# Kernel tuning notes

Hardware: AMD Instinct MI355X
Metric: run time of the kernel (lower is better)

Reference implementation:

```python
import jax, jax.numpy as jnp
import numpy as np

NEG_INF = -1e30  # stand-in for -inf, avoids NaN under masked rows edge cases


def setup_inputs() -> dict:
    key = jax.random.key(0)
    ks = jax.random.split(key, 6)
    H, N, F_IN, HD, F_OUT = 8, 4096, 512, 64, 512
    X = jax.random.normal(ks[0], (H, N, F_IN), dtype=jnp.float32)
    mask = jax.random.randint(ks[1], (H, N, N), 0, 2, dtype=jnp.int32)
    s = 1.0 / np.sqrt(F_IN)
    W_Q = jax.random.normal(ks[2], (H, HD, F_IN), dtype=jnp.float32) * s
    W_K = jax.random.normal(ks[3], (H, HD, F_IN), dtype=jnp.float32) * s
    W_V = jax.random.normal(ks[4], (H, HD, F_IN), dtype=jnp.float32) * s
    W_O = jax.random.normal(ks[5], (F_OUT, H * HD), dtype=jnp.float32) * (1.0 / np.sqrt(H * HD))
    return {"X": X, "mask": mask, "W_Q": W_Q, "W_K": W_K, "W_V": W_V, "W_O": W_O}


def reference(X, mask, W_Q, W_K, W_V, W_O):
    # X: [H, N, F_in]; W_{Q,K,V}: [H, head_dim, F_in] (torch Linear layout: [out,in])
    Q = jnp.einsum('hnf,hdf->hnd', X, W_Q)
    K = jnp.einsum('hnf,hdf->hnd', X, W_K)
    V = jnp.einsum('hnf,hdf->hnd', X, W_V)
    head_dim = K.shape[-1]
    E = jnp.einsum('hnd,hmd->hnm', Q, K) / jnp.sqrt(jnp.float32(head_dim))  # [H,N,N]
    E = jnp.where(mask == 0, jnp.float32(NEG_INF), E)
    A = jax.nn.softmax(E, axis=-1)
    Hout = jnp.einsum('hnm,hmd->hnd', A, V)  # [H, N, head_dim]
    # concat heads along feature dim -> [N, H*head_dim]
    Hcat = jnp.transpose(Hout, (1, 0, 2)).reshape(Hout.shape[1], -1)
    # dropout is identity in eval mode
    return Hcat @ W_O.T  # [N, fan_out]
```

## Files before the change

### kernel.cpp

```cpp
#include <hip/hip_runtime.h>

typedef __bf16 bf16x8 __attribute__((ext_vector_type(8)));
typedef float f32x4 __attribute__((ext_vector_type(4)));
typedef int i32x4 __attribute__((ext_vector_type(4)));

#define MFMA(a, b, c) __builtin_amdgcn_mfma_f32_16x16x32_bf16((a), (b), (c), 0, 0, 0)
#define GLOAD_LDS(g, l) __builtin_amdgcn_global_load_lds( \
    (const __attribute__((address_space(1))) void*)(g),   \
    (__attribute__((address_space(3))) void*)(l), 16, 0, 0)

constexpr int HEADS = 8, SEQ = 4096, FIN = 512, HD = 64, FOUT = 512;
constexpr float QSCALE = 0.18033688011112042f;

__device__ inline bf16x8 cvt8(const float* __restrict__ p) {
    f32x4 a = *(const f32x4*)p;
    f32x4 b = *(const f32x4*)(p + 4);
    bf16x8 r;
    r[0] = (__bf16)a[0]; r[1] = (__bf16)a[1]; r[2] = (__bf16)a[2]; r[3] = (__bf16)a[3];
    r[4] = (__bf16)b[0]; r[5] = (__bf16)b[1]; r[6] = (__bf16)b[2]; r[7] = (__bf16)b[3];
    return r;
}

__global__ __launch_bounds__(256) void qkv_kernel(
    const float* __restrict__ X, const float* __restrict__ Wq,
    const float* __restrict__ Wk, const float* __restrict__ Wv,
    __bf16* __restrict__ Q, __bf16* __restrict__ K, __bf16* __restrict__ Vt)
{
    const int h = blockIdx.y;
    const int tid = threadIdx.x;
    const int w = tid >> 6, lane = tid & 63;
    const int quad = lane >> 4, l16 = lane & 15;
    const int m = blockIdx.x * 64 + w * 16 + l16;

    const float* xrow = X + ((size_t)h * SEQ + m) * FIN + quad * 8;
    const float* wqh = Wq + (size_t)h * HD * FIN + quad * 8;
    const float* wkh = Wk + (size_t)h * HD * FIN + quad * 8;
    const float* wvh = Wv + (size_t)h * HD * FIN + quad * 8;

    const f32x4 vzero = {0.f, 0.f, 0.f, 0.f};
    f32x4 accQ[4], accK[4], accV[4];
#pragma unroll
    for (int t = 0; t < 4; ++t) { accQ[t] = vzero; accK[t] = vzero; accV[t] = vzero; }

    for (int f0 = 0; f0 < FIN; f0 += 32) {
        bf16x8 a = cvt8(xrow + f0);
#pragma unroll
        for (int t = 0; t < 4; ++t) {
            const int wrow = (t * 16 + l16) * FIN + f0;
            bf16x8 bq = cvt8(wqh + wrow);
            bf16x8 bk = cvt8(wkh + wrow);
            bf16x8 bv = cvt8(wvh + wrow);
            accQ[t] = MFMA(a, bq, accQ[t]);
            accK[t] = MFMA(a, bk, accK[t]);
            accV[t] = MFMA(a, bv, accV[t]);
        }
    }

    const int row0 = blockIdx.x * 64 + w * 16 + quad * 4;
#pragma unroll
    for (int t = 0; t < 4; ++t) {
        const int d = t * 16 + l16;
#pragma unroll
        for (int r = 0; r < 4; ++r) {
            const int n = row0 + r;
            Q[((size_t)h * SEQ + n) * HD + d] = (__bf16)(accQ[t][r] * QSCALE);
            K[((size_t)h * SEQ + n) * HD + d] = (__bf16)accK[t][r];
            Vt[((size_t)h * HD + d) * SEQ + n] = (__bf16)accV[t][r];
        }
    }
}

__global__ __launch_bounds__(256) void attn_kernel(
    const __bf16* __restrict__ Q, const __bf16* __restrict__ K,
    const __bf16* __restrict__ Vt, const int* __restrict__ mask,
    __bf16* __restrict__ Hcat)
{
    __shared__ __align__(16) unsigned char lds[32768 + 4 * 2048];

    const int bid = blockIdx.x;
    const int h = bid & 7;
    const int q0b = (bid >> 3) * 64;
    const int tid = threadIdx.x;
    const int w = tid >> 6, lane = tid & 63;
    const int quad = lane >> 4, l16 = lane & 15;
    const int q0 = q0b + w * 16;
    const int e7 = l16 & 7;

    __bf16* PT = (__bf16*)(lds + 32768) + w * 1024;

    const __bf16* Qh = Q + (size_t)h * SEQ * HD;
    const __bf16* Kh = K + (size_t)h * SEQ * HD;
    const __bf16* Vh = Vt + (size_t)h * HD * SEQ;
    const int* mrow = mask + ((size_t)h * SEQ + q0 + l16) * SEQ + quad * 4;

    auto stage = [&](int n0, int b) {
        unsigned char* bK = lds + b * 8192;
        unsigned char* bV = lds + 16384 + b * 8192;
#pragma unroll
        for (int c = 0; c < 2; ++c) {
            const int s = c * 256 + w * 64 + lane;
            const int row = s >> 3;
            const int cq = (s & 7) ^ (row & 7);
            GLOAD_LDS(Kh + (size_t)(n0 + row) * HD + cq * 8, bK + (c * 256 + w * 64) * 16);
            GLOAD_LDS(Vh + (size_t)row * SEQ + n0 + cq * 8, bV + (c * 256 + w * 64) * 16);
        }
    };
    auto loadM = [&](int n0, i32x4* mv) {
#pragma unroll
        for (int t = 0; t < 4; ++t) mv[t] = *(const i32x4*)(mrow + n0 + t * 16);
    };

    bf16x8 qa0 = *(const bf16x8*)(Qh + (size_t)(q0 + l16) * HD + quad * 8);
    bf16x8 qa1 = *(const bf16x8*)(Qh + (size_t)(q0 + l16) * HD + 32 + quad * 8);

    const f32x4 vzero = {0.f, 0.f, 0.f, 0.f};
    f32x4 O[4];
    float lsum = 0.f;
#pragma unroll
    for (int t = 0; t < 4; ++t) O[t] = vzero;

    i32x4 mA[4], mB[4];
    stage(0, 0);
    loadM(0, mA);
    __syncthreads();

    auto tile = [&](int i, const i32x4* mc, i32x4* mn) {
        const int n0 = i * 64;
        const int cur = i & 1;
        if (i + 1 < SEQ / 64) {
            stage(n0 + 64, cur ^ 1);
            loadM(n0 + 64, mn);
        }
        const __bf16* cK = (const __bf16*)(lds + cur * 8192);
        const __bf16* cV = (const __bf16*)(lds + 16384 + cur * 8192);

        f32x4 St[4];
#pragma unroll
        for (int t = 0; t < 4; ++t) {
            const int kr = t * 16 + l16;
            bf16x8 kb0 = *(const bf16x8*)(cK + kr * 64 + ((quad ^ (kr & 7)) * 8));
            bf16x8 kb1 = *(const bf16x8*)(cK + kr * 64 + (((quad + 4) ^ (kr & 7)) * 8));
            St[t] = MFMA(kb0, qa0, vzero);
            St[t] = MFMA(kb1, qa1, St[t]);
        }

#pragma unroll
        for (int t = 0; t < 4; ++t) {
            union { unsigned long long u; __bf16 hh[4]; } pk;
#pragma unroll
            for (int r = 0; r < 4; ++r) {
                float p = __builtin_amdgcn_exp2f(St[t][r]);
                p = mc[t][r] ? p : 0.f;
                lsum += p;
                pk.hh[r] = (__bf16)p;
            }
            const int c = t * 2 + (quad >> 1);
            *(unsigned long long*)(PT + l16 * 64 + ((c ^ e7) * 8) + (quad & 1) * 4) = pk.u;
        }

        bf16x8 pa0 = *(const bf16x8*)(PT + l16 * 64 + ((quad ^ e7) * 8));
        bf16x8 pa1 = *(const bf16x8*)(PT + l16 * 64 + (((quad + 4) ^ e7) * 8));
#pragma unroll
        for (int t = 0; t < 4; ++t) {
            const int dr = t * 16 + l16;
            bf16x8 vb0 = *(const bf16x8*)(cV + dr * 64 + ((quad ^ (dr & 7)) * 8));
            bf16x8 vb1 = *(const bf16x8*)(cV + dr * 64 + (((quad + 4) ^ (dr & 7)) * 8));
            O[t] = MFMA(pa0, vb0, O[t]);
            O[t] = MFMA(pa1, vb1, O[t]);
        }
        __syncthreads();
    };

    for (int i = 0; i < SEQ / 64; i += 2) {
        tile(i, mA, mB);
        tile(i + 1, mB, mA);
    }

    lsum += __shfl_xor(lsum, 16, 64);
    lsum += __shfl_xor(lsum, 32, 64);
    float inv[4];
#pragma unroll
    for (int r = 0; r < 4; ++r) {
        float Lr = __shfl(lsum, quad * 4 + r, 64);
        inv[r] = Lr > 0.f ? 1.0f / Lr : 0.f;
    }

#pragma unroll
    for (int r = 0; r < 4; ++r) {
        const int n = q0 + quad * 4 + r;
#pragma unroll
        for (int t = 0; t < 4; ++t)
            Hcat[(size_t)n * FOUT + h * HD + t * 16 + l16] = (__bf16)(O[t][r] * inv[r]);
    }
}

__global__ __launch_bounds__(256) void out_kernel(
    const __bf16* __restrict__ Hcat, const float* __restrict__ Wo,
    float* __restrict__ out)
{
    const int tid = threadIdx.x;
    const int w = tid >> 6, lane = tid & 63;
    const int quad = lane >> 4, l16 = lane & 15;
    const int n0 = blockIdx.x * 64 + w * 16;
    const int o0 = blockIdx.y * 64;

    const f32x4 vzero = {0.f, 0.f, 0.f, 0.f};
    f32x4 acc[4];
#pragma unroll
    for (int t = 0; t < 4; ++t) acc[t] = vzero;

    for (int k0 = 0; k0 < FOUT; k0 += 32) {
        bf16x8 a = *(const bf16x8*)(Hcat + (size_t)(n0 + l16) * FOUT + k0 + quad * 8);
#pragma unroll
        for (int t = 0; t < 4; ++t) {
            bf16x8 b = cvt8(Wo + (size_t)(o0 + t * 16 + l16) * FOUT + k0 + quad * 8);
            acc[t] = MFMA(a, b, acc[t]);
        }
    }
#pragma unroll
    for (int t = 0; t < 4; ++t)
#pragma unroll
        for (int r = 0; r < 4; ++r)
            out[(size_t)(n0 + quad * 4 + r) * FOUT + o0 + t * 16 + l16] = acc[t][r];
}

extern "C" void kernel_launch(void* const* d_in, const int* in_sizes, int n_in,
                              void* d_out, int out_size, void* d_ws, size_t ws_size,
                              hipStream_t stream) {
    const float* X    = (const float*)d_in[0];
    const int*   mask = (const int*)d_in[1];
    const float* Wq   = (const float*)d_in[2];
    const float* Wk   = (const float*)d_in[3];
    const float* Wv   = (const float*)d_in[4];
    const float* Wo   = (const float*)d_in[5];
    float* out = (float*)d_out;

    __bf16* Q    = (__bf16*)d_ws;
    __bf16* K    = Q + (size_t)HEADS * SEQ * HD;
    __bf16* Vt   = K + (size_t)HEADS * SEQ * HD;
    __bf16* Hcat = Vt + (size_t)HEADS * HD * SEQ;

    qkv_kernel<<<dim3(SEQ / 64, HEADS), 256, 0, stream>>>(X, Wq, Wk, Wv, Q, K, Vt);
    attn_kernel<<<(SEQ / 64) * HEADS, 256, 0, stream>>>(Q, K, Vt, mask, Hcat);
    out_kernel<<<dim3(SEQ / 64, FOUT / 64), 256, 0, stream>>>(Hcat, Wo, out);
}
```

Before: 895.2 us.

## Split attention key dimension in two with a separate combine kernel

```diff
diff --git a/kernel.cpp b/kernel.cpp
--- a/kernel.cpp
+++ b/kernel.cpp
@@ -10,6 +10,8 @@
     (__attribute__((address_space(3))) void*)(l), 16, 0, 0)
 
 constexpr int HEADS = 8, SEQ = 4096, FIN = 512, HD = 64, FOUT = 512;
+constexpr int KSPLIT = 2;
+constexpr int NT = SEQ / 64 / KSPLIT;
 constexpr float QSCALE = 0.18033688011112042f;
 
 __device__ inline bf16x8 cvt8(const float* __restrict__ p) {
@@ -73,13 +75,15 @@
 __global__ __launch_bounds__(256) void attn_kernel(
     const __bf16* __restrict__ Q, const __bf16* __restrict__ K,
     const __bf16* __restrict__ Vt, const int* __restrict__ mask,
-    __bf16* __restrict__ Hcat)
+    float* __restrict__ Opart, float* __restrict__ Lpart)
 {
     __shared__ __align__(16) unsigned char lds[32768 + 4 * 2048];
 
     const int bid = blockIdx.x;
     const int h = bid & 7;
-    const int q0b = (bid >> 3) * 64;
+    const int sp = (bid >> 3) & (KSPLIT - 1);
+    const int q0b = (bid >> 4) * 64;
+    const int nbase = sp * (SEQ / KSPLIT);
     const int tid = threadIdx.x;
     const int w = tid >> 6, lane = tid & 63;
     const int quad = lane >> 4, l16 = lane & 15;
@@ -120,14 +124,14 @@
     for (int t = 0; t < 4; ++t) O[t] = vzero;
 
     i32x4 mA[4], mB[4];
-    stage(0, 0);
-    loadM(0, mA);
+    stage(nbase, 0);
+    loadM(nbase, mA);
     __syncthreads();
 
     auto tile = [&](int i, const i32x4* mc, i32x4* mn) {
-        const int n0 = i * 64;
+        const int n0 = nbase + i * 64;
         const int cur = i & 1;
-        if (i + 1 < SEQ / 64) {
+        if (i + 1 < NT) {
             stage(n0 + 64, cur ^ 1);
             loadM(n0 + 64, mn);
         }
@@ -171,27 +175,46 @@
         __syncthreads();
     };
 
-    for (int i = 0; i < SEQ / 64; i += 2) {
+    for (int i = 0; i < NT; i += 2) {
         tile(i, mA, mB);
         tile(i + 1, mB, mA);
     }
 
     lsum += __shfl_xor(lsum, 16, 64);
     lsum += __shfl_xor(lsum, 32, 64);
-    float inv[4];
-#pragma unroll
-    for (int r = 0; r < 4; ++r) {
-        float Lr = __shfl(lsum, quad * 4 + r, 64);
-        inv[r] = Lr > 0.f ? 1.0f / Lr : 0.f;
-    }
-
+
+    float* Op = Opart + (size_t)(sp * HEADS + h) * SEQ * HD;
 #pragma unroll
     for (int r = 0; r < 4; ++r) {
         const int n = q0 + quad * 4 + r;
 #pragma unroll
         for (int t = 0; t < 4; ++t)
-            Hcat[(size_t)n * FOUT + h * HD + t * 16 + l16] = (__bf16)(O[t][r] * inv[r]);
-    }
+            Op[(size_t)n * HD + t * 16 + l16] = O[t][r];
+    }
+    if (quad == 0)
+        Lpart[(size_t)(sp * HEADS + h) * SEQ + q0 + l16] = lsum;
+}
+
+__global__ __launch_bounds__(256) void combine_kernel(
+    const float* __restrict__ Opart, const float* __restrict__ Lpart,
+    __bf16* __restrict__ Hcat)
+{
+    const int gid = blockIdx.x * 256 + threadIdx.x;
+    const int dq = gid & 15;
+    const int n = (gid >> 4) & (SEQ - 1);
+    const int h = gid >> 16;
+
+    const float* p0 = Opart + ((size_t)h * SEQ + n) * HD + dq * 4;
+    const float* p1 = p0 + (size_t)HEADS * SEQ * HD;
+    const float l = Lpart[(size_t)h * SEQ + n] + Lpart[(size_t)(HEADS + h) * SEQ + n];
+    const float inv = l > 0.f ? 1.0f / l : 0.f;
+
+    f32x4 a = *(const f32x4*)p0;
+    f32x4 b = *(const f32x4*)p1;
+    union { unsigned long long u; __bf16 hh[4]; } o;
+#pragma unroll
+    for (int j = 0; j < 4; ++j) o.hh[j] = (__bf16)((a[j] + b[j]) * inv);
+    *(unsigned long long*)(Hcat + (size_t)n * FOUT + h * HD + dq * 4) = o.u;
 }
 
 __global__ __launch_bounds__(256) void out_kernel(
@@ -239,8 +262,11 @@
     __bf16* K    = Q + (size_t)HEADS * SEQ * HD;
     __bf16* Vt   = K + (size_t)HEADS * SEQ * HD;
     __bf16* Hcat = Vt + (size_t)HEADS * HD * SEQ;
+    float* Opart = (float*)(Hcat + (size_t)SEQ * FOUT);
+    float* Lpart = Opart + (size_t)KSPLIT * HEADS * SEQ * HD;
 
     qkv_kernel<<<dim3(SEQ / 64, HEADS), 256, 0, stream>>>(X, Wq, Wk, Wv, Q, K, Vt);
-    attn_kernel<<<(SEQ / 64) * HEADS, 256, 0, stream>>>(Q, K, Vt, mask, Hcat);
+    attn_kernel<<<(SEQ / 64) * HEADS * KSPLIT, 256, 0, stream>>>(Q, K, Vt, mask, Opart, Lpart);
+    combine_kernel<<<HEADS * SEQ * 16 / 256, 256, 0, stream>>>(Opart, Lpart, Hcat);
     out_kernel<<<dim3(SEQ / 64, FOUT / 64), 256, 0, stream>>>(Hcat, Wo, out);
 }
```

New measurement: 905.7 us. Within noise of the previous version (+1.2%).

## Split attention key tiles across waves and reduce partial outputs in LDS

Applied to the files above, without the earlier changes.

```diff
diff --git a/kernel.cpp b/kernel.cpp
--- a/kernel.cpp
+++ b/kernel.cpp
@@ -75,7 +75,7 @@
     const __bf16* __restrict__ Vt, const int* __restrict__ mask,
     __bf16* __restrict__ Hcat)
 {
-    __shared__ __align__(16) unsigned char lds[32768 + 4 * 2048];
+    __shared__ __align__(16) unsigned char lds[4 * 64 * 68 * 4 + 4 * 64 * 4];
 
     const int bid = blockIdx.x;
     const int h = bid & 7;
@@ -83,15 +83,12 @@
     const int tid = threadIdx.x;
     const int w = tid >> 6, lane = tid & 63;
     const int quad = lane >> 4, l16 = lane & 15;
-    const int q0 = q0b + w * 16;
     const int e7 = l16 & 7;
-
-    __bf16* PT = (__bf16*)(lds + 32768) + w * 1024;
 
     const __bf16* Qh = Q + (size_t)h * SEQ * HD;
     const __bf16* Kh = K + (size_t)h * SEQ * HD;
     const __bf16* Vh = Vt + (size_t)h * HD * SEQ;
-    const int* mrow = mask + ((size_t)h * SEQ + q0 + l16) * SEQ + quad * 4;
+    const int* mbase = mask + ((size_t)h * SEQ + q0b + l16) * SEQ + w * 16 + quad * 4;
 
     auto stage = [&](int n0, int b) {
         unsigned char* bK = lds + b * 8192;
@@ -107,17 +104,23 @@
     };
     auto loadM = [&](int n0, i32x4* mv) {
 #pragma unroll
-        for (int t = 0; t < 4; ++t) mv[t] = *(const i32x4*)(mrow + n0 + t * 16);
+        for (int g = 0; g < 4; ++g) mv[g] = *(const i32x4*)(mbase + g * (16 * SEQ) + n0);
     };
 
-    bf16x8 qa0 = *(const bf16x8*)(Qh + (size_t)(q0 + l16) * HD + quad * 8);
-    bf16x8 qa1 = *(const bf16x8*)(Qh + (size_t)(q0 + l16) * HD + 32 + quad * 8);
+    bf16x8 qa[4][2];
+#pragma unroll
+    for (int g = 0; g < 4; ++g)
+#pragma unroll
+        for (int c = 0; c < 2; ++c)
+            qa[g][c] = *(const bf16x8*)(Qh + (size_t)(q0b + g * 16 + l16) * HD + c * 32 + quad * 8);
 
     const f32x4 vzero = {0.f, 0.f, 0.f, 0.f};
-    f32x4 O[4];
-    float lsum = 0.f;
-#pragma unroll
-    for (int t = 0; t < 4; ++t) O[t] = vzero;
+    f32x4 O[4][4];
+    float ls[4] = {0.f, 0.f, 0.f, 0.f};
+#pragma unroll
+    for (int g = 0; g < 4; ++g)
+#pragma unroll
+        for (int u = 0; u < 4; ++u) O[g][u] = vzero;
 
     i32x4 mA[4], mB[4];
     stage(0, 0);
@@ -134,40 +137,46 @@
         const __bf16* cK = (const __bf16*)(lds + cur * 8192);
         const __bf16* cV = (const __bf16*)(lds + 16384 + cur * 8192);
 
+        const int krow = w * 16 + l16;
+        bf16x8 kb0 = *(const bf16x8*)(cK + krow * 64 + ((quad ^ e7) * 8));
+        bf16x8 kb1 = *(const bf16x8*)(cK + krow * 64 + (((quad + 4) ^ e7) * 8));
+
         f32x4 St[4];
-#pragma unroll
-        for (int t = 0; t < 4; ++t) {
-            const int kr = t * 16 + l16;
-            bf16x8 kb0 = *(const bf16x8*)(cK + kr * 64 + ((quad ^ (kr & 7)) * 8));
-            bf16x8 kb1 = *(const bf16x8*)(cK + kr * 64 + (((quad + 4) ^ (kr & 7)) * 8));
-            St[t] = MFMA(kb0, qa0, vzero);
-            St[t] = MFMA(kb1, qa1, St[t]);
-        }
-
-#pragma unroll
-        for (int t = 0; t < 4; ++t) {
-            union { unsigned long long u; __bf16 hh[4]; } pk;
+        __builtin_amdgcn_s_setprio(1);
+#pragma unroll
+        for (int g = 0; g < 4; ++g) {
+            St[g] = MFMA(kb0, qa[g][0], vzero);
+            St[g] = MFMA(kb1, qa[g][1], St[g]);
+        }
+        __builtin_amdgcn_s_setprio(0);
+
+        bf16x8 pa[4];
+#pragma unroll
+        for (int g = 0; g < 4; ++g) {
+            bf16x8 z = {};
 #pragma unroll
             for (int r = 0; r < 4; ++r) {
-                float p = __builtin_amdgcn_exp2f(St[t][r]);
-                p = mc[t][r] ? p : 0.f;
-                lsum += p;
-                pk.hh[r] = (__bf16)p;
+                float p = __builtin_amdgcn_exp2f(St[g][r]);
+                p = mc[g][r] ? p : 0.f;
+                ls[g] += p;
+                z[r] = (__bf16)p;
             }
-            const int c = t * 2 + (quad >> 1);
-            *(unsigned long long*)(PT + l16 * 64 + ((c ^ e7) * 8) + (quad & 1) * 4) = pk.u;
-        }
-
-        bf16x8 pa0 = *(const bf16x8*)(PT + l16 * 64 + ((quad ^ e7) * 8));
-        bf16x8 pa1 = *(const bf16x8*)(PT + l16 * 64 + (((quad + 4) ^ e7) * 8));
-#pragma unroll
-        for (int t = 0; t < 4; ++t) {
-            const int dr = t * 16 + l16;
-            bf16x8 vb0 = *(const bf16x8*)(cV + dr * 64 + ((quad ^ (dr & 7)) * 8));
-            bf16x8 vb1 = *(const bf16x8*)(cV + dr * 64 + (((quad + 4) ^ (dr & 7)) * 8));
-            O[t] = MFMA(pa0, vb0, O[t]);
-            O[t] = MFMA(pa1, vb1, O[t]);
-        }
+            pa[g] = z;
+        }
+
+        __builtin_amdgcn_s_setprio(1);
+        const int vslot = (w * 2 + (quad >> 1)) ^ e7;
+        const int vsub = (quad & 1) * 4;
+#pragma unroll
+        for (int u = 0; u < 4; ++u) {
+            bf16x8 vb = {};
+            *(unsigned long long*)&vb =
+                *(const unsigned long long*)(cV + (u * 16 + l16) * 64 + vslot * 8 + vsub);
+#pragma unroll
+            for (int g = 0; g < 4; ++g)
+                O[g][u] = MFMA(pa[g], vb, O[g][u]);
+        }
+        __builtin_amdgcn_s_setprio(0);
         __syncthreads();
     };
 
@@ -176,22 +185,45 @@
         tile(i + 1, mB, mA);
     }
 
-    lsum += __shfl_xor(lsum, 16, 64);
-    lsum += __shfl_xor(lsum, 32, 64);
-    float inv[4];
-#pragma unroll
-    for (int r = 0; r < 4; ++r) {
-        float Lr = __shfl(lsum, quad * 4 + r, 64);
-        inv[r] = Lr > 0.f ? 1.0f / Lr : 0.f;
-    }
-
-#pragma unroll
-    for (int r = 0; r < 4; ++r) {
-        const int n = q0 + quad * 4 + r;
-#pragma unroll
-        for (int t = 0; t < 4; ++t)
-            Hcat[(size_t)n * FOUT + h * HD + t * 16 + l16] = (__bf16)(O[t][r] * inv[r]);
-    }
+    float* Ored = (float*)lds;
+    float* Lred = (float*)(lds + 4 * 64 * 68 * 4);
+    float* myO = Ored + w * (64 * 68);
+#pragma unroll
+    for (int g = 0; g < 4; ++g) {
+#pragma unroll
+        for (int u = 0; u < 4; ++u)
+#pragma unroll
+            for (int r = 0; r < 4; ++r)
+                myO[(g * 16 + quad * 4 + r) * 68 + u * 16 + l16] = O[g][u][r];
+        float s = ls[g];
+        s += __shfl_xor(s, 16, 64);
+        s += __shfl_xor(s, 32, 64);
+        if (lane < 16) Lred[w * 64 + g * 16 + lane] = s;
+    }
+    __syncthreads();
+
+    const int q = tid >> 2, d0 = (tid & 3) * 16;
+    const float l = Lred[q] + Lred[64 + q] + Lred[128 + q] + Lred[192 + q];
+    const float inv = l > 0.f ? 1.0f / l : 0.f;
+    float acc[16];
+#pragma unroll
+    for (int v = 0; v < 4; ++v) {
+        f32x4 s = *(const f32x4*)(Ored + q * 68 + d0 + v * 4);
+#pragma unroll
+        for (int w2 = 1; w2 < 4; ++w2)
+            s += *(const f32x4*)(Ored + w2 * (64 * 68) + q * 68 + d0 + v * 4);
+#pragma unroll
+        for (int j = 0; j < 4; ++j) acc[v * 4 + j] = s[j];
+    }
+    bf16x8 o0, o1;
+#pragma unroll
+    for (int j = 0; j < 8; ++j) {
+        o0[j] = (__bf16)(acc[j] * inv);
+        o1[j] = (__bf16)(acc[8 + j] * inv);
+    }
+    __bf16* dst = Hcat + (size_t)(q0b + q) * FOUT + h * HD + d0;
+    *(bf16x8*)dst = o0;
+    *(bf16x8*)(dst + 8) = o1;
 }
 
 __global__ __launch_bounds__(256) void out_kernel(
```

Measured after the change: 914.3 us. 2.1% more time.
